# Kernel optimization log

Measured on AMD Instinct MI355X. Metric: run time of the kernel, lower is better.

## Reference

```python
import jax, jax.numpy as jnp
import numpy as np
import math

B, S, F_IN = 8, 1024, 32
D, H, L, NCLS = 512, 8, 6, 3
DFF = 4 * D
DK = D // H
EPS = 1e-5


def make_pe(max_len, d_model):
    pos = jnp.arange(max_len, dtype=jnp.float32)[:, None]
    div = jnp.exp(jnp.arange(0, d_model, 2, dtype=jnp.float32) * (-math.log(10000.0) / d_model))
    pe = jnp.zeros((max_len, d_model), dtype=jnp.float32)
    pe = pe.at[:, 0::2].set(jnp.sin(pos * div))
    pe = pe.at[:, 1::2].set(jnp.cos(pos * div))
    return pe  # [max_len, D]


def layernorm(x, g, b):
    m = jnp.mean(x, -1, keepdims=True)
    v = jnp.mean((x - m) ** 2, -1, keepdims=True)
    return (x - m) * jax.lax.rsqrt(v + EPS) * g + b


def setup_inputs() -> dict:
    key = jax.random.key(0)
    ks = iter(jax.random.split(key, 40))

    def w(shape, scale=None):
        k = next(ks)
        s = scale if scale is not None else 1.0 / math.sqrt(shape[0])
        return jax.random.normal(k, shape, dtype=jnp.float32) * s

    inp = {
        'x': jax.random.normal(next(ks), (B, S, F_IN), dtype=jnp.float32),
        'pe': make_pe(S, D),
        'emb_w': w((F_IN, D)), 'emb_b': jnp.zeros((D,), jnp.float32),
        'Wq': w((L, D, D)), 'bq': jnp.zeros((L, D), jnp.float32),
        'Wk': w((L, D, D)), 'bk': jnp.zeros((L, D), jnp.float32),
        'Wv': w((L, D, D)), 'bv': jnp.zeros((L, D), jnp.float32),
        'Wo': w((L, D, D)), 'bo': jnp.zeros((L, D), jnp.float32),
        'ln1_g': jnp.ones((L, D), jnp.float32), 'ln1_b': jnp.zeros((L, D), jnp.float32),
        'ln2_g': jnp.ones((L, D), jnp.float32), 'ln2_b': jnp.zeros((L, D), jnp.float32),
        'W1': w((L, D, DFF)), 'b1': jnp.zeros((L, DFF), jnp.float32),
        'W2': w((L, DFF, D)), 'b2': jnp.zeros((L, D), jnp.float32),
        'fc1_w': w((D, 256)), 'fc1_b': jnp.zeros((256,), jnp.float32),
        'fc2_w': w((256, 128)), 'fc2_b': jnp.zeros((128,), jnp.float32),
        'fc3_w': w((128, NCLS)), 'fc3_b': jnp.zeros((NCLS,), jnp.float32),
    }
    return inp


def reference(x, pe, emb_w, emb_b, Wq, bq, Wk, bk, Wv, bv, Wo, bo,
              ln1_g, ln1_b, ln2_g, ln2_b, W1, b1, W2, b2,
              fc1_w, fc1_b, fc2_w, fc2_b, fc3_w, fc3_b):
    scale = math.sqrt(DK)
    h = x @ emb_w + emb_b                      # [B,S,D]
    h = h + pe[None, :S, :]                    # positional encoding
    for l in range(L):
        # multi-head self-attention (full O(S^2) scores, as in source)
        q = (h @ Wq[l] + bq[l]).reshape(B, S, H, DK).transpose(0, 2, 1, 3)
        k = (h @ Wk[l] + bk[l]).reshape(B, S, H, DK).transpose(0, 2, 1, 3)
        v = (h @ Wv[l] + bv[l]).reshape(B, S, H, DK).transpose(0, 2, 1, 3)
        scores = jnp.einsum('bhqd,bhkd->bhqk', q, k) / scale   # [B,H,S,S]
        attn = jax.nn.softmax(scores, axis=-1)
        ctx = jnp.einsum('bhqk,bhkd->bhqd', attn, v)           # [B,H,S,DK]
        ctx = ctx.transpose(0, 2, 1, 3).reshape(B, S, D)
        attn_out = ctx @ Wo[l] + bo[l]
        h = layernorm(h + attn_out, ln1_g[l], ln1_b[l])
        ff = jax.nn.relu(h @ W1[l] + b1[l]) @ W2[l] + b2[l]
        h = layernorm(h + ff, ln2_g[l], ln2_b[l])
    pooled = jnp.mean(h, axis=1)               # AdaptiveAvgPool1d(1) over seq
    z = jax.nn.relu(pooled @ fc1_w + fc1_b)
    z = jax.nn.relu(z @ fc2_w + fc2_b)
    return z @ fc3_w + fc3_b                   # [B, NCLS]
```

## Files before the change

### kernel.cpp

```cpp
#include <hip/hip_runtime.h>
#include <math.h>

#define B_   8
#define S_   1024
#define FIN  32
#define D_   512
#define H_   8
#define L_   6
#define DFF_ 2048
#define DK_  64

__device__ __forceinline__ float mulrn(float a, float b) { return __fmul_rn(a, b); }
__device__ __forceinline__ float addrn(float a, float b) { return __fadd_rn(a, b); }

__global__ __launch_bounds__(128) void k_embed(const float* __restrict__ x,
                                               const float* __restrict__ emb_w,
                                               const float* __restrict__ emb_b,
                                               const float* __restrict__ pe,
                                               float* __restrict__ h) {
    int row = blockIdx.x;
    int s = row & (S_ - 1);
    int t = threadIdx.x;
    __shared__ float xs[FIN];
    if (t < FIN) xs[t] = x[row * FIN + t];
    __syncthreads();
    int d = t * 4;
    float a0 = 0.f, a1 = 0.f, a2 = 0.f, a3 = 0.f;
#pragma unroll
    for (int k = 0; k < FIN; ++k) {
        float xv = xs[k];
        const float* wr = &emb_w[k * D_ + d];
        a0 = fmaf(xv, wr[0], a0);
        a1 = fmaf(xv, wr[1], a1);
        a2 = fmaf(xv, wr[2], a2);
        a3 = fmaf(xv, wr[3], a3);
    }
    const float* bb = &emb_b[d];
    const float* pp = &pe[s * D_ + d];
    float4 o;
    o.x = addrn(addrn(a0, bb[0]), pp[0]);
    o.y = addrn(addrn(a1, bb[1]), pp[1]);
    o.z = addrn(addrn(a2, bb[2]), pp[2]);
    o.w = addrn(addrn(a3, bb[3]), pp[3]);
    *(float4*)&h[(size_t)row * D_ + d] = o;
}

template<bool RELU>
__global__ __launch_bounds__(256) void k_gemm(const float* __restrict__ A,
                                              const float* __restrict__ W,
                                              const float* __restrict__ bias,
                                              float* __restrict__ C,
                                              int M, int N, int K) {
    __shared__ float As[2][16][68];
    __shared__ float Bs[2][16][68];
    int bm = blockIdx.y * 64, bn = blockIdx.x * 64;
    int t = threadIdx.x;
    int tr = t >> 4, tc = t & 15;
    int ar = t >> 2, ak = (t & 3) * 4;
    int wk = t >> 4, wn = (t & 15) * 4;
    float acc[4][4] = {};

    float4 pa = *(const float4*)&A[(size_t)(bm + ar) * K + ak];
    float4 pw = *(const float4*)&W[(size_t)wk * N + bn + wn];
    As[0][ak + 0][ar] = pa.x; As[0][ak + 1][ar] = pa.y;
    As[0][ak + 2][ar] = pa.z; As[0][ak + 3][ar] = pa.w;
    *(float4*)&Bs[0][wk][wn] = pw;
    __syncthreads();

    const int nP = K >> 4;
    for (int p = 0; p < nP; ++p) {
        int cur = p & 1;
        if (p + 1 < nP) {
            pa = *(const float4*)&A[(size_t)(bm + ar) * K + (p + 1) * 16 + ak];
            pw = *(const float4*)&W[(size_t)((p + 1) * 16 + wk) * N + bn + wn];
        }
#pragma unroll
        for (int kk = 0; kk < 16; ++kk) {
            float4 av = *(const float4*)&As[cur][kk][tr * 4];
            float4 bv = *(const float4*)&Bs[cur][kk][tc * 4];
            acc[0][0] = fmaf(av.x, bv.x, acc[0][0]); acc[0][1] = fmaf(av.x, bv.y, acc[0][1]);
            acc[0][2] = fmaf(av.x, bv.z, acc[0][2]); acc[0][3] = fmaf(av.x, bv.w, acc[0][3]);
            acc[1][0] = fmaf(av.y, bv.x, acc[1][0]); acc[1][1] = fmaf(av.y, bv.y, acc[1][1]);
            acc[1][2] = fmaf(av.y, bv.z, acc[1][2]); acc[1][3] = fmaf(av.y, bv.w, acc[1][3]);
            acc[2][0] = fmaf(av.z, bv.x, acc[2][0]); acc[2][1] = fmaf(av.z, bv.y, acc[2][1]);
            acc[2][2] = fmaf(av.z, bv.z, acc[2][2]); acc[2][3] = fmaf(av.z, bv.w, acc[2][3]);
            acc[3][0] = fmaf(av.w, bv.x, acc[3][0]); acc[3][1] = fmaf(av.w, bv.y, acc[3][1]);
            acc[3][2] = fmaf(av.w, bv.z, acc[3][2]); acc[3][3] = fmaf(av.w, bv.w, acc[3][3]);
        }
        if (p + 1 < nP) {
            int nxt = cur ^ 1;
            As[nxt][ak + 0][ar] = pa.x; As[nxt][ak + 1][ar] = pa.y;
            As[nxt][ak + 2][ar] = pa.z; As[nxt][ak + 3][ar] = pa.w;
            *(float4*)&Bs[nxt][wk][wn] = pw;
        }
        __syncthreads();
    }
    float4 b4 = *(const float4*)&bias[bn + tc * 4];
#pragma unroll
    for (int i = 0; i < 4; ++i) {
        float4 o;
        o.x = addrn(acc[i][0], b4.x); o.y = addrn(acc[i][1], b4.y);
        o.z = addrn(acc[i][2], b4.z); o.w = addrn(acc[i][3], b4.w);
        if (RELU) {
            o.x = fmaxf(o.x, 0.f); o.y = fmaxf(o.y, 0.f);
            o.z = fmaxf(o.z, 0.f); o.w = fmaxf(o.w, 0.f);
        }
        *(float4*)&C[(size_t)(bm + tr * 4 + i) * N + bn + tc * 4] = o;
    }
}

__global__ __launch_bounds__(256) void k_attn(const float* q,
                                              const float* __restrict__ kg,
                                              const float* __restrict__ vg,
                                              float* ctx) {
    __shared__ float KVs[32][68];
    __shared__ float Ss[64 * 276];
    int hh = blockIdx.x;
    int ch = blockIdx.y;
    int b  = blockIdx.z;
    int t  = threadIdx.x;
    int r  = t >> 4, c16 = t & 15;
    const int row0 = ch * 16;
    const size_t base = (size_t)b * S_ * D_ + hh * DK_;
    const int srr = t >> 4, scc = (t & 15) * 4;

    *(float4*)&KVs[srr][scc] = *(const float4*)&q[base + (size_t)(row0 + srr) * D_ + scc];
    __syncthreads();
    float4 qr[16];
#pragma unroll
    for (int i = 0; i < 16; ++i) qr[i] = *(float4*)&KVs[r][i * 4];

    float4 nx0 = *(const float4*)&kg[base + (size_t)srr * D_ + scc];
    float4 nx1 = *(const float4*)&kg[base + (size_t)(srr + 16) * D_ + scc];
    __syncthreads();
    *(float4*)&KVs[srr][scc] = nx0;
    *(float4*)&KVs[srr + 16][scc] = nx1;
    __syncthreads();
    for (int kt = 0; kt < 32; ++kt) {
        if (kt < 31) {
            size_t rowb = base + (size_t)((kt + 1) * 32) * D_;
            nx0 = *(const float4*)&kg[rowb + (size_t)srr * D_ + scc];
            nx1 = *(const float4*)&kg[rowb + (size_t)(srr + 16) * D_ + scc];
        }
        float s0 = 0.f, s1 = 0.f;
#pragma unroll
        for (int d4 = 0; d4 < 16; ++d4) {
            float4 qv = qr[d4];
            float4 k0 = *(float4*)&KVs[c16][d4 * 4];
            float4 k1 = *(float4*)&KVs[c16 + 16][d4 * 4];
            s0 = addrn(s0, mulrn(qv.x, k0.x)); s1 = addrn(s1, mulrn(qv.x, k1.x));
            s0 = addrn(s0, mulrn(qv.y, k0.y)); s1 = addrn(s1, mulrn(qv.y, k1.y));
            s0 = addrn(s0, mulrn(qv.z, k0.z)); s1 = addrn(s1, mulrn(qv.z, k1.z));
            s0 = addrn(s0, mulrn(qv.w, k0.w)); s1 = addrn(s1, mulrn(qv.w, k1.w));
        }
        int jg0 = kt * 32 + c16;
        int jg1 = jg0 + 16;
        Ss[(jg0 & 63) * 276 + (jg0 >> 6) * 17 + r] = mulrn(s0, 0.125f);
        Ss[(jg1 & 63) * 276 + (jg1 >> 6) * 17 + r] = mulrn(s1, 0.125f);
        __syncthreads();
        if (kt < 31) {
            *(float4*)&KVs[srr][scc] = nx0;
            *(float4*)&KVs[srr + 16][scc] = nx1;
            __syncthreads();
        }
    }

    const int rbase = c16 * 17 + r;
    float mx = -INFINITY;
#pragma unroll
    for (int jj = 0; jj < 64; ++jj)
        mx = fmaxf(mx, Ss[jj * 276 + rbase]);
    mx = fmaxf(mx, __shfl_xor(mx, 1));
    mx = fmaxf(mx, __shfl_xor(mx, 2));
    mx = fmaxf(mx, __shfl_xor(mx, 4));
    mx = fmaxf(mx, __shfl_xor(mx, 8));

    float psum = 0.f;
#pragma unroll
    for (int jj = 0; jj < 64; ++jj) {
        float p = expf(__fsub_rn(Ss[jj * 276 + rbase], mx));
        Ss[jj * 276 + rbase] = p;
        psum = addrn(psum, p);
    }
    psum = addrn(psum, __shfl_xor(psum, 1));
    psum = addrn(psum, __shfl_xor(psum, 2));
    psum = addrn(psum, __shfl_xor(psum, 4));
    psum = addrn(psum, __shfl_xor(psum, 8));
#pragma unroll
    for (int jj = 0; jj < 64; ++jj)
        Ss[jj * 276 + rbase] = __fdiv_rn(Ss[jj * 276 + rbase], psum);

    int d0 = c16 * 4;
    float a0 = 0.f, a1 = 0.f, a2 = 0.f, a3 = 0.f;
    nx0 = *(const float4*)&vg[base + (size_t)srr * D_ + scc];
    nx1 = *(const float4*)&vg[base + (size_t)(srr + 16) * D_ + scc];
    __syncthreads();
    *(float4*)&KVs[srr][scc] = nx0;
    *(float4*)&KVs[srr + 16][scc] = nx1;
    __syncthreads();
    for (int vt = 0; vt < 32; ++vt) {
        if (vt < 31) {
            size_t rowb = base + (size_t)((vt + 1) * 32) * D_;
            nx0 = *(const float4*)&vg[rowb + (size_t)srr * D_ + scc];
            nx1 = *(const float4*)&vg[rowb + (size_t)(srr + 16) * D_ + scc];
        }
        const float* srow = &Ss[(vt & 1) * 32 * 276 + (vt >> 1) * 17 + r];
#pragma unroll
        for (int jl = 0; jl < 32; ++jl) {
            float p = srow[jl * 276];
            float4 v4 = *(float4*)&KVs[jl][d0];
            a0 = addrn(a0, mulrn(p, v4.x));
            a1 = addrn(a1, mulrn(p, v4.y));
            a2 = addrn(a2, mulrn(p, v4.z));
            a3 = addrn(a3, mulrn(p, v4.w));
        }
        __syncthreads();
        if (vt < 31) {
            *(float4*)&KVs[srr][scc] = nx0;
            *(float4*)&KVs[srr + 16][scc] = nx1;
            __syncthreads();
        }
    }
    float4 o = {a0, a1, a2, a3};
    *(float4*)&ctx[base + (size_t)(row0 + r) * D_ + d0] = o;
}

__global__ __launch_bounds__(256) void k_add_ln(float* h,
                                                const float* __restrict__ res,
                                                const float* __restrict__ g,
                                                const float* __restrict__ bta) {
    int row = blockIdx.x;
    int t = threadIdx.x;
    size_t base = (size_t)row * D_;
    float y0 = addrn(h[base + t],       res[base + t]);
    float y1 = addrn(h[base + t + 256], res[base + t + 256]);
    __shared__ float red[4];
    int w = t >> 6;
    float s = y0 + y1;
#pragma unroll
    for (int o = 1; o < 64; o <<= 1) s += __shfl_xor(s, o);
    if ((t & 63) == 0) red[w] = s;
    __syncthreads();
    float mean = (red[0] + red[1] + red[2] + red[3]) * (1.f / D_);
    __syncthreads();
    float d0 = __fsub_rn(y0, mean), d1 = __fsub_rn(y1, mean);
    s = mulrn(d0, d0) + mulrn(d1, d1);
#pragma unroll
    for (int o = 1; o < 64; o <<= 1) s += __shfl_xor(s, o);
    if ((t & 63) == 0) red[w] = s;
    __syncthreads();
    float var = (red[0] + red[1] + red[2] + red[3]) * (1.f / D_);
    float rstd = __fdiv_rn(1.0f, sqrtf(__fadd_rn(var, 1e-5f)));
    h[base + t]       = addrn(mulrn(mulrn(d0, rstd), g[t]),       bta[t]);
    h[base + t + 256] = addrn(mulrn(mulrn(d1, rstd), g[t + 256]), bta[t + 256]);
}

__global__ __launch_bounds__(256) void k_pool(const float* __restrict__ h,
                                              float* __restrict__ pooled) {
    int blk = blockIdx.x;
    int b = blk >> 3, dc = (blk & 7) * 64;
    int t = threadIdx.x;
    int d = dc + (t & 63), sg = t >> 6;
    float s = 0.f;
    for (int ss = sg; ss < S_; ss += 4)
        s = addrn(s, h[((size_t)b * S_ + ss) * D_ + d]);
    __shared__ float sh[4][64];
    sh[sg][t & 63] = s;
    __syncthreads();
    if (t < 64)
        pooled[b * D_ + dc + t] = (sh[0][t] + sh[1][t] + sh[2][t] + sh[3][t]) * (1.f / S_);
}

__global__ __launch_bounds__(256) void k_head(const float* __restrict__ pooled,
                                              const float* __restrict__ w1, const float* __restrict__ b1,
                                              const float* __restrict__ w2, const float* __restrict__ b2,
                                              const float* __restrict__ w3, const float* __restrict__ b3,
                                              float* __restrict__ out) {
    __shared__ float ps[B_][D_];
    __shared__ float z1[B_][256];
    __shared__ float z2[B_][128];
    int t = threadIdx.x;
    for (int i = t; i < B_ * D_; i += 256) ps[i >> 9][i & 511] = pooled[i];
    __syncthreads();
    {
        float acc[B_] = {};
        for (int k = 0; k < D_; ++k) {
            float w = w1[k * 256 + t];
#pragma unroll
            for (int b = 0; b < B_; ++b) acc[b] = fmaf(ps[b][k], w, acc[b]);
        }
#pragma unroll
        for (int b = 0; b < B_; ++b) z1[b][t] = fmaxf(addrn(acc[b], b1[t]), 0.f);
    }
    __syncthreads();
    if (t < 128) {
        float acc[B_] = {};
        for (int k = 0; k < 256; ++k) {
            float w = w2[k * 128 + t];
#pragma unroll
            for (int b = 0; b < B_; ++b) acc[b] = fmaf(z1[b][k], w, acc[b]);
        }
#pragma unroll
        for (int b = 0; b < B_; ++b) z2[b][t] = fmaxf(addrn(acc[b], b2[t]), 0.f);
    }
    __syncthreads();
    if (t < B_ * 3) {
        int b = t / 3, c = t % 3;
        float acc = 0.f;
        for (int k = 0; k < 128; ++k) acc = fmaf(z2[b][k], w3[k * 3 + c], acc);
        out[t] = addrn(acc, b3[c]);
    }
}

extern "C" void kernel_launch(void* const* d_in, const int* in_sizes, int n_in,
                              void* d_out, int out_size, void* d_ws, size_t ws_size,
                              hipStream_t stream) {
    const float* x     = (const float*)d_in[0];
    const float* pe    = (const float*)d_in[1];
    const float* emb_w = (const float*)d_in[2];
    const float* emb_b = (const float*)d_in[3];
    const float* Wq    = (const float*)d_in[4];
    const float* bq    = (const float*)d_in[5];
    const float* Wk    = (const float*)d_in[6];
    const float* bk    = (const float*)d_in[7];
    const float* Wv    = (const float*)d_in[8];
    const float* bv    = (const float*)d_in[9];
    const float* Wo    = (const float*)d_in[10];
    const float* bo    = (const float*)d_in[11];
    const float* ln1_g = (const float*)d_in[12];
    const float* ln1_b = (const float*)d_in[13];
    const float* ln2_g = (const float*)d_in[14];
    const float* ln2_b = (const float*)d_in[15];
    const float* W1    = (const float*)d_in[16];
    const float* b1    = (const float*)d_in[17];
    const float* W2    = (const float*)d_in[18];
    const float* b2    = (const float*)d_in[19];
    const float* fc1_w = (const float*)d_in[20];
    const float* fc1_b = (const float*)d_in[21];
    const float* fc2_w = (const float*)d_in[22];
    const float* fc2_b = (const float*)d_in[23];
    const float* fc3_w = (const float*)d_in[24];
    const float* fc3_b = (const float*)d_in[25];

    const size_t NBS = (size_t)B_ * S_ * D_;
    float* ws = (float*)d_ws;
    const int MROWS = B_ * S_;

    float* h = ws;
    float* q = h + NBS;
    float* k = q + NBS;
    float* v = k + NBS;
    float* pooled = v + NBS;

    k_embed<<<MROWS, 128, 0, stream>>>(x, emb_w, emb_b, pe, h);

    dim3 g512(D_ / 64, MROWS / 64);
    dim3 gff(DFF_ / 64, 4096 / 64);
    dim3 gw2(D_ / 64, 4096 / 64);
    dim3 gattn(H_, S_ / 16, B_);

    for (int l = 0; l < L_; ++l) {
        const float* wq = Wq + (size_t)l * D_ * D_;
        const float* wk = Wk + (size_t)l * D_ * D_;
        const float* wv = Wv + (size_t)l * D_ * D_;
        const float* wo = Wo + (size_t)l * D_ * D_;
        k_gemm<false><<<g512, 256, 0, stream>>>(h, wq, bq + l * D_, q, MROWS, D_, D_);
        k_gemm<false><<<g512, 256, 0, stream>>>(h, wk, bk + l * D_, k, MROWS, D_, D_);
        k_gemm<false><<<g512, 256, 0, stream>>>(h, wv, bv + l * D_, v, MROWS, D_, D_);
        k_attn<<<gattn, 256, 0, stream>>>(q, k, v, q);
        k_gemm<false><<<g512, 256, 0, stream>>>(q, wo, bo + l * D_, k, MROWS, D_, D_);
        k_add_ln<<<MROWS, 256, 0, stream>>>(h, k, ln1_g + l * D_, ln1_b + l * D_);
        for (int c = 0; c < 2; ++c) {
            float* ff1 = q;
            k_gemm<true ><<<gff, 256, 0, stream>>>(h + (size_t)c * 4096 * D_,
                W1 + (size_t)l * D_ * DFF_, b1 + l * DFF_, ff1, 4096, DFF_, D_);
            k_gemm<false><<<gw2, 256, 0, stream>>>(ff1,
                W2 + (size_t)l * DFF_ * D_, b2 + l * D_, v + (size_t)c * 4096 * D_, 4096, D_, DFF_);
        }
        k_add_ln<<<MROWS, 256, 0, stream>>>(h, v, ln2_g + l * D_, ln2_b + l * D_);
    }

    k_pool<<<B_ * 8, 256, 0, stream>>>(h, pooled);
    k_head<<<1, 256, 0, stream>>>(pooled, fc1_w, fc1_b, fc2_w, fc2_b, fc3_w, fc3_b, (float*)d_out);
}
```

Measured before the change: 7.321 ms.

## Use 128-row GEMM tiles and deepen K/V prefetch in attention

Adds a 128x64 tiled GEMM kernel where each thread computes an 8x4 block, and uses it for the QKV, output and first FFN projections; the second FFN GEMM keeps the 64x64 kernel. This raises arithmetic per shared-memory load and halves the number of blocks. The attention kernel now prefetches K and V tiles two iterations ahead into registers instead of one, to hide global load latency. The extra registers may lower occupancy, and the 512-block grids may underfill the GPU.

```diff
diff --git a/kernel.cpp b/kernel.cpp
--- a/kernel.cpp
+++ b/kernel.cpp
@@ -46,11 +46,11 @@
 }
 
 template<bool RELU>
-__global__ __launch_bounds__(256) void k_gemm(const float* __restrict__ A,
-                                              const float* __restrict__ W,
-                                              const float* __restrict__ bias,
-                                              float* __restrict__ C,
-                                              int M, int N, int K) {
+__global__ __launch_bounds__(256) void k_gemm64(const float* __restrict__ A,
+                                                const float* __restrict__ W,
+                                                const float* __restrict__ bias,
+                                                float* __restrict__ C,
+                                                int M, int N, int K) {
     __shared__ float As[2][16][68];
     __shared__ float Bs[2][16][68];
     int bm = blockIdx.y * 64, bn = blockIdx.x * 64;
@@ -106,6 +106,86 @@
             o.z = fmaxf(o.z, 0.f); o.w = fmaxf(o.w, 0.f);
         }
         *(float4*)&C[(size_t)(bm + tr * 4 + i) * N + bn + tc * 4] = o;
+    }
+}
+
+template<bool RELU>
+__global__ __launch_bounds__(256) void k_gemm128(const float* __restrict__ A,
+                                                 const float* __restrict__ W,
+                                                 const float* __restrict__ bias,
+                                                 float* __restrict__ C,
+                                                 int M, int N, int K) {
+    __shared__ float As[2][16][132];
+    __shared__ float Bs[2][16][68];
+    int bm = blockIdx.y * 128, bn = blockIdx.x * 64;
+    int t = threadIdx.x;
+    int tr = t >> 4, tc = t & 15;
+    int a0r = t >> 2,        a0k = (t & 3) * 4;
+    int a1r = (256 + t) >> 2, a1k = a0k;
+    int wk = t >> 4, wn = (t & 15) * 4;
+    float acc[8][4] = {};
+
+    float4 pa0 = *(const float4*)&A[(size_t)(bm + a0r) * K + a0k];
+    float4 pa1 = *(const float4*)&A[(size_t)(bm + a1r) * K + a1k];
+    float4 pw  = *(const float4*)&W[(size_t)wk * N + bn + wn];
+    As[0][a0k + 0][a0r] = pa0.x; As[0][a0k + 1][a0r] = pa0.y;
+    As[0][a0k + 2][a0r] = pa0.z; As[0][a0k + 3][a0r] = pa0.w;
+    As[0][a1k + 0][a1r] = pa1.x; As[0][a1k + 1][a1r] = pa1.y;
+    As[0][a1k + 2][a1r] = pa1.z; As[0][a1k + 3][a1r] = pa1.w;
+    *(float4*)&Bs[0][wk][wn] = pw;
+    __syncthreads();
+
+    const int nP = K >> 4;
+    for (int p = 0; p < nP; ++p) {
+        int cur = p & 1;
+        if (p + 1 < nP) {
+            pa0 = *(const float4*)&A[(size_t)(bm + a0r) * K + (p + 1) * 16 + a0k];
+            pa1 = *(const float4*)&A[(size_t)(bm + a1r) * K + (p + 1) * 16 + a1k];
+            pw  = *(const float4*)&W[(size_t)((p + 1) * 16 + wk) * N + bn + wn];
+        }
+#pragma unroll
+        for (int kk = 0; kk < 16; ++kk) {
+            float4 av0 = *(const float4*)&As[cur][kk][tr * 8];
+            float4 av1 = *(const float4*)&As[cur][kk][tr * 8 + 4];
+            float4 bv  = *(const float4*)&Bs[cur][kk][tc * 4];
+            acc[0][0] = fmaf(av0.x, bv.x, acc[0][0]); acc[0][1] = fmaf(av0.x, bv.y, acc[0][1]);
+            acc[0][2] = fmaf(av0.x, bv.z, acc[0][2]); acc[0][3] = fmaf(av0.x, bv.w, acc[0][3]);
+            acc[1][0] = fmaf(av0.y, bv.x, acc[1][0]); acc[1][1] = fmaf(av0.y, bv.y, acc[1][1]);
+            acc[1][2] = fmaf(av0.y, bv.z, acc[1][2]); acc[1][3] = fmaf(av0.y, bv.w, acc[1][3]);
+            acc[2][0] = fmaf(av0.z, bv.x, acc[2][0]); acc[2][1] = fmaf(av0.z, bv.y, acc[2][1]);
+            acc[2][2] = fmaf(av0.z, bv.z, acc[2][2]); acc[2][3] = fmaf(av0.z, bv.w, acc[2][3]);
+            acc[3][0] = fmaf(av0.w, bv.x, acc[3][0]); acc[3][1] = fmaf(av0.w, bv.y, acc[3][1]);
+            acc[3][2] = fmaf(av0.w, bv.z, acc[3][2]); acc[3][3] = fmaf(av0.w, bv.w, acc[3][3]);
+            acc[4][0] = fmaf(av1.x, bv.x, acc[4][0]); acc[4][1] = fmaf(av1.x, bv.y, acc[4][1]);
+            acc[4][2] = fmaf(av1.x, bv.z, acc[4][2]); acc[4][3] = fmaf(av1.x, bv.w, acc[4][3]);
+            acc[5][0] = fmaf(av1.y, bv.x, acc[5][0]); acc[5][1] = fmaf(av1.y, bv.y, acc[5][1]);
+            acc[5][2] = fmaf(av1.y, bv.z, acc[5][2]); acc[5][3] = fmaf(av1.y, bv.w, acc[5][3]);
+            acc[6][0] = fmaf(av1.z, bv.x, acc[6][0]); acc[6][1] = fmaf(av1.z, bv.y, acc[6][1]);
+            acc[6][2] = fmaf(av1.z, bv.z, acc[6][2]); acc[6][3] = fmaf(av1.z, bv.w, acc[6][3]);
+            acc[7][0] = fmaf(av1.w, bv.x, acc[7][0]); acc[7][1] = fmaf(av1.w, bv.y, acc[7][1]);
+            acc[7][2] = fmaf(av1.w, bv.z, acc[7][2]); acc[7][3] = fmaf(av1.w, bv.w, acc[7][3]);
+        }
+        if (p + 1 < nP) {
+            int nxt = cur ^ 1;
+            As[nxt][a0k + 0][a0r] = pa0.x; As[nxt][a0k + 1][a0r] = pa0.y;
+            As[nxt][a0k + 2][a0r] = pa0.z; As[nxt][a0k + 3][a0r] = pa0.w;
+            As[nxt][a1k + 0][a1r] = pa1.x; As[nxt][a1k + 1][a1r] = pa1.y;
+            As[nxt][a1k + 2][a1r] = pa1.z; As[nxt][a1k + 3][a1r] = pa1.w;
+            *(float4*)&Bs[nxt][wk][wn] = pw;
+        }
+        __syncthreads();
+    }
+    float4 b4 = *(const float4*)&bias[bn + tc * 4];
+#pragma unroll
+    for (int i = 0; i < 8; ++i) {
+        float4 o;
+        o.x = addrn(acc[i][0], b4.x); o.y = addrn(acc[i][1], b4.y);
+        o.z = addrn(acc[i][2], b4.z); o.w = addrn(acc[i][3], b4.w);
+        if (RELU) {
+            o.x = fmaxf(o.x, 0.f); o.y = fmaxf(o.y, 0.f);
+            o.z = fmaxf(o.z, 0.f); o.w = fmaxf(o.w, 0.f);
+        }
+        *(float4*)&C[(size_t)(bm + tr * 8 + i) * N + bn + tc * 4] = o;
     }
 }
 
@@ -130,17 +210,23 @@
 #pragma unroll
     for (int i = 0; i < 16; ++i) qr[i] = *(float4*)&KVs[r][i * 4];
 
-    float4 nx0 = *(const float4*)&kg[base + (size_t)srr * D_ + scc];
-    float4 nx1 = *(const float4*)&kg[base + (size_t)(srr + 16) * D_ + scc];
-    __syncthreads();
-    *(float4*)&KVs[srr][scc] = nx0;
-    *(float4*)&KVs[srr + 16][scc] = nx1;
+    float4 nA0 = *(const float4*)&kg[base + (size_t)srr * D_ + scc];
+    float4 nA1 = *(const float4*)&kg[base + (size_t)(srr + 16) * D_ + scc];
+    float4 nB0, nB1;
+    __syncthreads();
+    *(float4*)&KVs[srr][scc] = nA0;
+    *(float4*)&KVs[srr + 16][scc] = nA1;
+    {
+        size_t rowb = base + (size_t)32 * D_;
+        nA0 = *(const float4*)&kg[rowb + (size_t)srr * D_ + scc];
+        nA1 = *(const float4*)&kg[rowb + (size_t)(srr + 16) * D_ + scc];
+    }
     __syncthreads();
     for (int kt = 0; kt < 32; ++kt) {
-        if (kt < 31) {
-            size_t rowb = base + (size_t)((kt + 1) * 32) * D_;
-            nx0 = *(const float4*)&kg[rowb + (size_t)srr * D_ + scc];
-            nx1 = *(const float4*)&kg[rowb + (size_t)(srr + 16) * D_ + scc];
+        if (kt < 30) {
+            size_t rowb = base + (size_t)((kt + 2) * 32) * D_;
+            nB0 = *(const float4*)&kg[rowb + (size_t)srr * D_ + scc];
+            nB1 = *(const float4*)&kg[rowb + (size_t)(srr + 16) * D_ + scc];
         }
         float s0 = 0.f, s1 = 0.f;
 #pragma unroll
@@ -159,10 +245,11 @@
         Ss[(jg1 & 63) * 276 + (jg1 >> 6) * 17 + r] = mulrn(s1, 0.125f);
         __syncthreads();
         if (kt < 31) {
-            *(float4*)&KVs[srr][scc] = nx0;
-            *(float4*)&KVs[srr + 16][scc] = nx1;
+            *(float4*)&KVs[srr][scc] = nA0;
+            *(float4*)&KVs[srr + 16][scc] = nA1;
             __syncthreads();
         }
+        nA0 = nB0; nA1 = nB1;
     }
 
     const int rbase = c16 * 17 + r;
@@ -192,17 +279,22 @@
 
     int d0 = c16 * 4;
     float a0 = 0.f, a1 = 0.f, a2 = 0.f, a3 = 0.f;
-    nx0 = *(const float4*)&vg[base + (size_t)srr * D_ + scc];
-    nx1 = *(const float4*)&vg[base + (size_t)(srr + 16) * D_ + scc];
-    __syncthreads();
-    *(float4*)&KVs[srr][scc] = nx0;
-    *(float4*)&KVs[srr + 16][scc] = nx1;
+    nA0 = *(const float4*)&vg[base + (size_t)srr * D_ + scc];
+    nA1 = *(const float4*)&vg[base + (size_t)(srr + 16) * D_ + scc];
+    __syncthreads();
+    *(float4*)&KVs[srr][scc] = nA0;
+    *(float4*)&KVs[srr + 16][scc] = nA1;
+    {
+        size_t rowb = base + (size_t)32 * D_;
+        nA0 = *(const float4*)&vg[rowb + (size_t)srr * D_ + scc];
+        nA1 = *(const float4*)&vg[rowb + (size_t)(srr + 16) * D_ + scc];
+    }
     __syncthreads();
     for (int vt = 0; vt < 32; ++vt) {
-        if (vt < 31) {
-            size_t rowb = base + (size_t)((vt + 1) * 32) * D_;
-            nx0 = *(const float4*)&vg[rowb + (size_t)srr * D_ + scc];
-            nx1 = *(const float4*)&vg[rowb + (size_t)(srr + 16) * D_ + scc];
+        if (vt < 30) {
+            size_t rowb = base + (size_t)((vt + 2) * 32) * D_;
+            nB0 = *(const float4*)&vg[rowb + (size_t)srr * D_ + scc];
+            nB1 = *(const float4*)&vg[rowb + (size_t)(srr + 16) * D_ + scc];
         }
         const float* srow = &Ss[(vt & 1) * 32 * 276 + (vt >> 1) * 17 + r];
 #pragma unroll
@@ -216,10 +308,11 @@
         }
         __syncthreads();
         if (vt < 31) {
-            *(float4*)&KVs[srr][scc] = nx0;
-            *(float4*)&KVs[srr + 16][scc] = nx1;
+            *(float4*)&KVs[srr][scc] = nA0;
+            *(float4*)&KVs[srr + 16][scc] = nA1;
             __syncthreads();
         }
+        nA0 = nB0; nA1 = nB1;
     }
     float4 o = {a0, a1, a2, a3};
     *(float4*)&ctx[base + (size_t)(row0 + r) * D_ + d0] = o;
@@ -354,8 +447,8 @@
 
     k_embed<<<MROWS, 128, 0, stream>>>(x, emb_w, emb_b, pe, h);
 
-    dim3 g512(D_ / 64, MROWS / 64);
-    dim3 gff(DFF_ / 64, 4096 / 64);
+    dim3 g512(D_ / 64, MROWS / 128);
+    dim3 gff(DFF_ / 64, 4096 / 128);
     dim3 gw2(D_ / 64, 4096 / 64);
     dim3 gattn(H_, S_ / 16, B_);
 
@@ -364,17 +457,17 @@
         const float* wk = Wk + (size_t)l * D_ * D_;
         const float* wv = Wv + (size_t)l * D_ * D_;
         const float* wo = Wo + (size_t)l * D_ * D_;
-        k_gemm<false><<<g512, 256, 0, stream>>>(h, wq, bq + l * D_, q, MROWS, D_, D_);
-        k_gemm<false><<<g512, 256, 0, stream>>>(h, wk, bk + l * D_, k, MROWS, D_, D_);
-        k_gemm<false><<<g512, 256, 0, stream>>>(h, wv, bv + l * D_, v, MROWS, D_, D_);
+        k_gemm128<false><<<g512, 256, 0, stream>>>(h, wq, bq + l * D_, q, MROWS, D_, D_);
+        k_gemm128<false><<<g512, 256, 0, stream>>>(h, wk, bk + l * D_, k, MROWS, D_, D_);
+        k_gemm128<false><<<g512, 256, 0, stream>>>(h, wv, bv + l * D_, v, MROWS, D_, D_);
         k_attn<<<gattn, 256, 0, stream>>>(q, k, v, q);
-        k_gemm<false><<<g512, 256, 0, stream>>>(q, wo, bo + l * D_, k, MROWS, D_, D_);
+        k_gemm128<false><<<g512, 256, 0, stream>>>(q, wo, bo + l * D_, k, MROWS, D_, D_);
         k_add_ln<<<MROWS, 256, 0, stream>>>(h, k, ln1_g + l * D_, ln1_b + l * D_);
         for (int c = 0; c < 2; ++c) {
             float* ff1 = q;
-            k_gemm<true ><<<gff, 256, 0, stream>>>(h + (size_t)c * 4096 * D_,
+            k_gemm128<true ><<<gff, 256, 0, stream>>>(h + (size_t)c * 4096 * D_,
                 W1 + (size_t)l * D_ * DFF_, b1 + l * DFF_, ff1, 4096, DFF_, D_);
-            k_gemm<false><<<gw2, 256, 0, stream>>>(ff1,
+            k_gemm64<false><<<gw2, 256, 0, stream>>>(ff1,
                 W2 + (size_t)l * DFF_ * D_, b2 + l * D_, v + (size_t)c * 4096 * D_, 4096, D_, DFF_);
         }
         k_add_ln<<<MROWS, 256, 0, stream>>>(h, v, ln2_g + l * D_, ln2_b + l * D_);
```

New measurement: 7.950 ms. 8.6% more time.
